# Performance work log

Hardware: AMD Instinct MI355X
Metric: run time of the kernel (lower is better)

The kernel has to match this reference:

```python
import jax, jax.numpy as jnp
import numpy as np

B, S, NX, H = 8, 1024, 1024, 16
HD = NX // H  # head dim = 64
MASKED_BIAS = -10000.0


def setup_inputs() -> dict:
    key = jax.random.key(0)
    ks = jax.random.split(key, 6)
    return {
        "x": jax.random.normal(ks[0], (B, S, NX), dtype=jnp.float32),
        "query": jax.random.normal(ks[1], (B, S, NX), dtype=jnp.float32),
        "c_attn_w": jax.random.normal(ks[2], (NX, 3 * NX), dtype=jnp.float32) * 0.02,
        "c_attn_b": jnp.zeros((3 * NX,), dtype=jnp.float32),
        "c_proj_w": jax.random.normal(ks[3], (NX, NX), dtype=jnp.float32) * 0.02,
        "c_proj_b": jnp.zeros((NX,), dtype=jnp.float32),
    }


def _split_heads(t):
    # [B, S, NX] -> [B, H, S, HD]
    b, s, _ = t.shape
    return t.reshape(b, s, H, HD).transpose(0, 2, 1, 3)


def reference(x, query, c_attn_w, c_attn_b, c_proj_w, c_proj_b):
    # Conv1D: y = x @ W + b
    kv = x @ c_attn_w + c_attn_b          # [B,S,3NX]; use key/value slices
    qy = query @ c_attn_w + c_attn_b      # [B,S,3NX]; use query slice
    q = _split_heads(qy[..., :NX])                     # [B,H,S,HD]
    k = _split_heads(kv[..., NX:2 * NX])               # [B,H,S,HD]
    v = _split_heads(kv[..., 2 * NX:])                 # [B,H,S,HD]

    w = jnp.einsum("bhqd,bhkd->bhqk", q, k) / jnp.sqrt(jnp.float32(HD))
    causal = jnp.tril(jnp.ones((S, S), dtype=bool))[None, None]
    w = jnp.where(causal, w, jnp.float32(MASKED_BIAS))
    w = jax.nn.softmax(w, axis=-1)
    a = jnp.einsum("bhqk,bhkd->bhqd", w, v)            # [B,H,S,HD]
    a = a.transpose(0, 2, 1, 3).reshape(B, S, NX)      # merge heads
    return a @ c_proj_w + c_proj_b
```

## Files before the change

kernel.cpp:

```cpp
#include <hip/hip_runtime.h>
#include <cstdint>
#include <cstddef>

#define Bb   8
#define Ss   1024
#define NXx  1024
#define Hh   16
#define HDd  64
#define Mm   (Bb*Ss)

typedef __bf16 bf16x8 __attribute__((ext_vector_type(8)));
typedef float  f32x4  __attribute__((ext_vector_type(4)));

__device__ __forceinline__ unsigned short f2bf(float f) {
    union { float f; unsigned int u; } v; v.f = f;
    return (unsigned short)((v.u + 0x8000u) >> 16);
}
__device__ __forceinline__ unsigned int f2bf_hi(float f) {
    union { float f; unsigned int u; } v; v.f = f;
    return (v.u + 0x8000u) & 0xffff0000u;
}

__device__ __forceinline__ void load_lds16(const unsigned short* g, unsigned short* lds_base) {
    __builtin_amdgcn_global_load_lds(
        (const __attribute__((address_space(1))) void*)g,
        (__attribute__((address_space(3))) void*)lds_base, 16, 0, 0);
}

__global__ __launch_bounds__(256) void prep(
    const float* __restrict__ x, const float* __restrict__ query,
    const float* __restrict__ caw, const float* __restrict__ cpw,
    unsigned short* __restrict__ xb, unsigned short* __restrict__ qb,
    unsigned short* __restrict__ Wt, unsigned short* __restrict__ Pt)
{
    __shared__ float tile[32][33];
    const int bid = blockIdx.x;
    const int tid = threadIdx.x;

    if (bid < 16384) {
        const float* in = (bid < 8192) ? x : query;
        unsigned short* out = (bid < 8192) ? xb : qb;
        const int i = ((bid & 8191) * 256 + tid) * 4;
        const float4 v = *(const float4*)(in + i);
        unsigned long long p = (unsigned long long)f2bf(v.x)
            | ((unsigned long long)f2bf(v.y) << 16)
            | ((unsigned long long)f2bf(v.z) << 32)
            | ((unsigned long long)f2bf(v.w) << 48);
        *(unsigned long long*)(out + i) = p;
        return;
    }

    const float* in;
    unsigned short* out;
    int C, t;
    if (bid < 16384 + 3072) { in = caw; out = Wt; C = 3072; t = bid - 16384; }
    else                    { in = cpw; out = Pt; C = 1024; t = bid - 19456; }
    const int ntx = C >> 5;
    const int c0 = (t % ntx) * 32, r0 = (t / ntx) * 32;
    const int tx = tid & 31, ty = tid >> 5;
    for (int i = ty; i < 32; i += 8)
        tile[i][tx] = in[(size_t)(r0 + i) * C + c0 + tx];
    __syncthreads();
    for (int i = ty; i < 32; i += 8)
        out[(size_t)(c0 + i) * 1024 + r0 + tx] = f2bf(tile[tx][i]);
}

__global__ __launch_bounds__(256) void gemm128(
    const unsigned short* __restrict__ Ax,
    const unsigned short* __restrict__ Aq,
    const unsigned short* __restrict__ Bt,
    const float* __restrict__ bias,
    int K, int mode,
    unsigned short* __restrict__ out_q,
    unsigned short* __restrict__ out_k,
    unsigned short* __restrict__ out_v,
    float* __restrict__ out_f)
{
    __shared__ unsigned short smem[16384];
    unsigned short (*As)[64] = (unsigned short (*)[64])(smem);
    unsigned short (*Bs)[64] = (unsigned short (*)[64])(smem + 8192);

    const int tid  = threadIdx.x;
    const int w    = tid >> 6;
    const int lane = tid & 63;

    const int nx   = (mode == 0) ? 24 : 8;
    const int nxh  = nx >> 1;
    const int n    = blockIdx.x;
    const int xcd  = n & 7;
    const int sgrp = n >> 3;
    const int m0   = ((xcd >> 1) * 16 + sgrp / nxh) * 128;
    const int n0   = ((xcd & 1) * nxh + sgrp % nxh) * 128;
    const int region = n0 >> 10;
    const unsigned short* A = (mode == 0 && region == 0) ? Aq : Ax;

    const int wm   = (w >> 1) * 64;
    const int wn   = (w & 1) * 64;
    const int lrow = lane & 15;
    const int quad = lane >> 4;

    f32x4 acc[4][4] = {};

    const int rr   = lane >> 3;
    const int scol = (((lane & 7) ^ (lane >> 3)) << 3);
    const unsigned short* Ag = A  + (size_t)(m0 + w * 32 + rr) * K + scol;
    const unsigned short* Bg = Bt + (size_t)(n0 + w * 32 + rr) * K + scol;
    unsigned short* ldsA = smem + (w * 32) * 64;
    unsigned short* ldsB = smem + 8192 + (w * 32) * 64;

    const int swz = lrow & 7;

    for (int k0 = 0; k0 < K; k0 += 64) {
        __syncthreads();
#pragma unroll
        for (int c = 0; c < 4; ++c) {
            load_lds16(Ag + (size_t)(c * 8) * K + k0, ldsA + c * 512);
            load_lds16(Bg + (size_t)(c * 8) * K + k0, ldsB + c * 512);
        }
        __syncthreads();
#pragma unroll
        for (int kk = 0; kk < 2; ++kk) {
            bf16x8 af[4], bfr[4];
            const int pc = (((kk * 4 + quad) ^ swz) << 3);
#pragma unroll
            for (int i = 0; i < 4; ++i) {
                af[i]  = *(const bf16x8*)&As[wm + i * 16 + lrow][pc];
                bfr[i] = *(const bf16x8*)&Bs[wn + i * 16 + lrow][pc];
            }
#pragma unroll
            for (int i = 0; i < 4; ++i)
#pragma unroll
                for (int j = 0; j < 4; ++j)
                    acc[i][j] = __builtin_amdgcn_mfma_f32_16x16x32_bf16(af[i], bfr[j], acc[i][j], 0, 0, 0);
        }
    }

    __syncthreads();

    if (mode == 1) {
#pragma unroll
        for (int i = 0; i < 4; ++i)
#pragma unroll
            for (int j = 0; j < 4; ++j) {
                const int ncol = n0 + wn + j * 16 + lrow;
                const float bv = bias[ncol];
#pragma unroll
                for (int r = 0; r < 4; ++r) {
                    const int mrow = m0 + wm + i * 16 + quad * 4 + r;
                    out_f[(size_t)mrow * NXx + ncol] = acc[i][j][r] + bv;
                }
            }
        return;
    }

    unsigned short* ep = smem + w * 2048;

    if (region != 2) {
        unsigned short* outp = (region == 0) ? out_q : out_k;
#pragma unroll
        for (int j = 0; j < 4; ++j) {
            const float bv = bias[n0 + wn + j * 16 + lrow];
#pragma unroll
            for (int i = 0; i < 4; ++i)
#pragma unroll
                for (int r = 0; r < 4; ++r)
                    ep[(i * 16 + quad * 4 + r) * 24 + lrow] = f2bf(acc[i][j][r] + bv);
#pragma unroll
            for (int t = 0; t < 2; ++t) {
                const int c    = t * 64 + lane;
                const int row  = c >> 1, ch = (c & 1) * 8;
                const int mrow = m0 + wm + row;
                const int cc   = (n0 + wn + j * 16 + ch) & (NXx - 1);
                const int hh   = cc >> 6, dd = cc & 63;
                const int bh   = (mrow >> 10) * Hh + hh;
                const int ss   = mrow & (Ss - 1);
                *(uint4*)&outp[((size_t)bh * Ss + ss) * HDd + dd] =
                    *(const uint4*)&ep[row * 24 + ch];
            }
        }
    } else {
#pragma unroll
        for (int j = 0; j < 4; ++j) {
            const float bv = bias[n0 + wn + j * 16 + lrow];
#pragma unroll
            for (int i = 0; i < 4; ++i)
#pragma unroll
                for (int r = 0; r < 4; ++r)
                    ep[lrow * 72 + i * 16 + quad * 4 + r] = f2bf(acc[i][j][r] + bv);
#pragma unroll
            for (int t = 0; t < 2; ++t) {
                const int c    = t * 64 + lane;
                const int col  = c >> 3, rc = (c & 7) * 8;
                const int cc   = (n0 + wn + j * 16 + col) & (NXx - 1);
                const int hh   = cc >> 6, dd = cc & 63;
                const int mrow = m0 + wm + rc;
                const int bh   = (mrow >> 10) * Hh + hh;
                const int ss   = mrow & (Ss - 1);
                *(uint4*)&out_v[((size_t)bh * HDd + dd) * Ss + ss] =
                    *(const uint4*)&ep[col * 72 + rc];
            }
        }
    }
}

__global__ __launch_bounds__(512, 4) void gemm256(
    const unsigned short* __restrict__ Ax,
    const unsigned short* __restrict__ Aq,
    const unsigned short* __restrict__ Bt,
    const float* __restrict__ bias,
    unsigned short* __restrict__ out_q,
    unsigned short* __restrict__ out_k,
    unsigned short* __restrict__ out_v)
{
    __shared__ unsigned short lds[36864];

    const int tid  = threadIdx.x;
    const int w    = tid >> 6;
    const int lane = tid & 63;
    const int wm   = (w >> 1) * 64;
    const int wn   = (w & 1) * 64;
    const int lrow = lane & 15;
    const int quad = lane >> 4;
    const int ph   = (quad ^ (lrow & 3) ^ (lrow >> 2)) & 3;

    const int n    = blockIdx.x;
    const int xcd  = n & 7;
    const int sg   = n >> 3;
    const int mi   = (xcd >> 1) * 8 + sg / 12;
    const int ni   = (xcd & 1) * 12 + sg % 12;
    const int m0   = mi << 8;
    const int n0   = ni << 7;
    const int region = n0 >> 10;
    const unsigned short* A = (region == 0) ? Aq : Ax;

    const int srow = lane >> 2;
    const int scol = (((lane & 3) ^ (srow & 3) ^ ((srow >> 2) & 3)) << 3);
    const unsigned short* pA0 = A  + (size_t)(m0 + w * 32 + srow) * 1024 + scol;
    const unsigned short* pA1 = A  + (size_t)(m0 + w * 32 + 16 + srow) * 1024 + scol;
    const unsigned short* pB0 = Bt + (size_t)(n0 + w * 16 + srow) * 1024 + scol;

    f32x4 acc[4][4] = {};

#pragma unroll
    for (int p = 0; p < 2; ++p) {
        const int bb = p * 12288;
        load_lds16(pA0, lds + bb + w * 1024);
        load_lds16(pA1, lds + bb + w * 1024 + 512);
        load_lds16(pB0, lds + bb + 8192 + w * 512);
        pA0 += 32; pA1 += 32; pB0 += 32;
    }

    int cbuf = 0;
    int sbuf = 2;
#pragma unroll 1
    for (int t = 0; t < 32; ++t) {
        __builtin_amdgcn_s_barrier();
        asm volatile("" ::: "memory");
        if (t <= 29) {
            const int bb = sbuf * 12288;
            load_lds16(pA0, lds + bb + w * 1024);
            load_lds16(pA1, lds + bb + w * 1024 + 512);
            load_lds16(pB0, lds + bb + 8192 + w * 512);
            pA0 += 32; pA1 += 32; pB0 += 32;
            asm volatile("s_waitcnt vmcnt(6)" ::: "memory");
        } else if (t == 30) {
            asm volatile("s_waitcnt vmcnt(3)" ::: "memory");
        } else {
            asm volatile("s_waitcnt vmcnt(0)" ::: "memory");
        }
        __builtin_amdgcn_s_barrier();
        asm volatile("" ::: "memory");

        const int rA = cbuf * 12288 + (wm + lrow) * 32 + ph * 8;
        const int rB = cbuf * 12288 + 8192 + (wn + lrow) * 32 + ph * 8;
        bf16x8 af[4], bq[4];
#pragma unroll
        for (int i = 0; i < 4; ++i) af[i] = *(const bf16x8*)&lds[rA + i * 512];
#pragma unroll
        for (int j = 0; j < 4; ++j) bq[j] = *(const bf16x8*)&lds[rB + j * 512];
        __builtin_amdgcn_s_setprio(1);
#pragma unroll
        for (int i = 0; i < 4; ++i)
#pragma unroll
            for (int j = 0; j < 4; ++j)
                acc[i][j] = __builtin_amdgcn_mfma_f32_16x16x32_bf16(af[i], bq[j], acc[i][j], 0, 0, 0);
        __builtin_amdgcn_s_setprio(0);

        cbuf = (cbuf == 2) ? 0 : cbuf + 1;
        sbuf = (sbuf == 2) ? 0 : sbuf + 1;
    }

    __syncthreads();

    unsigned short* ep = lds + w * 2048;

    if (region != 2) {
        unsigned short* outp = (region == 0) ? out_q : out_k;
#pragma unroll
        for (int j = 0; j < 4; ++j) {
            const float bv = bias[n0 + wn + j * 16 + lrow];
#pragma unroll
            for (int i = 0; i < 4; ++i)
#pragma unroll
                for (int r = 0; r < 4; ++r)
                    ep[(i * 16 + quad * 4 + r) * 24 + lrow] = f2bf(acc[i][j][r] + bv);
#pragma unroll
            for (int tt = 0; tt < 2; ++tt) {
                const int c    = tt * 64 + lane;
                const int row  = c >> 1, ch = (c & 1) * 8;
                const int mrow = m0 + wm + row;
                const int cc   = (n0 + wn + j * 16 + ch) & (NXx - 1);
                const int hh   = cc >> 6, dd = cc & 63;
                const int bh   = (mrow >> 10) * Hh + hh;
                const int ss   = mrow & (Ss - 1);
                *(uint4*)&outp[((size_t)bh * Ss + ss) * HDd + dd] =
                    *(const uint4*)&ep[row * 24 + ch];
            }
        }
    } else {
#pragma unroll
        for (int j = 0; j < 4; ++j) {
            const float bv = bias[n0 + wn + j * 16 + lrow];
#pragma unroll
            for (int i = 0; i < 4; ++i)
#pragma unroll
                for (int r = 0; r < 4; ++r)
                    ep[lrow * 72 + i * 16 + quad * 4 + r] = f2bf(acc[i][j][r] + bv);
#pragma unroll
            for (int tt = 0; tt < 2; ++tt) {
                const int c    = tt * 64 + lane;
                const int col  = c >> 3, rc = (c & 7) * 8;
                const int cc   = (n0 + wn + j * 16 + col) & (NXx - 1);
                const int hh   = cc >> 6, dd = cc & 63;
                const int mrow = m0 + wm + rc;
                const int bh   = (mrow >> 10) * Hh + hh;
                const int ss   = mrow & (Ss - 1);
                *(uint4*)&out_v[((size_t)bh * HDd + dd) * Ss + ss] =
                    *(const uint4*)&ep[col * 72 + rc];
            }
        }
    }
}

__global__ __launch_bounds__(256) void flash_attn(
    const unsigned short* __restrict__ Qh,
    const unsigned short* __restrict__ Kh,
    const unsigned short* __restrict__ Vt,
    unsigned short* __restrict__ about)
{
    __shared__ unsigned short Ks[64][64];
    __shared__ unsigned short Vs[64][64];
    __shared__ unsigned short Pl[4][32][72];

    const int tid  = threadIdx.x;
    const int w    = tid >> 6;
    const int lane = tid & 63;
    const int bh   = blockIdx.x & 127;
    const int pr   = blockIdx.x >> 7;
    const int b    = bh >> 4, h = bh & 15;
    const int lrow = lane & 15;
    const int quad = lane >> 4;

    const unsigned short* Qb = Qh + (size_t)bh * Ss * HDd;
    const unsigned short* Kb = Kh + (size_t)bh * Ss * HDd;
    const unsigned short* Vb = Vt + (size_t)bh * HDd * Ss;

    const int sr = lane >> 3;
    const int lc = (((lane & 7) ^ (lane >> 3)) << 3);
    unsigned short* ldsK0 = &Ks[w * 16][0];
    unsigned short* ldsK1 = &Ks[w * 16 + 8][0];
    unsigned short* ldsV0 = &Vs[w * 16][0];
    unsigned short* ldsV1 = &Vs[w * 16 + 8][0];

    const int swz = lrow & 7;
    const int ca = ((quad ^ swz) << 3);
    const int cb = (((4 + quad) ^ swz) << 3);

    for (int half = 0; half < 2; ++half) {
        const int qt = half ? (7 - pr) : pr;
        const int qw = qt * 128 + w * 32;

        bf16x8 aq[2][2];
#pragma unroll
        for (int g = 0; g < 2; ++g)
#pragma unroll
            for (int c = 0; c < 2; ++c)
                aq[g][c] = *(const bf16x8*)(Qb + (size_t)(qw + g * 16 + lrow) * HDd + c * 32 + quad * 8);

        f32x4 O[2][4] = {};
        float lsum[2] = { 0.f, 0.f };

        const int nkt = 2 * qt + 2;
        for (int kt = 0; kt < nkt; ++kt) {
            const int k0 = kt * 64;

            __syncthreads();
            load_lds16(Kb + (size_t)(k0 + w * 16 + sr) * HDd + lc,     ldsK0);
            load_lds16(Kb + (size_t)(k0 + w * 16 + sr + 8) * HDd + lc, ldsK1);
            load_lds16(Vb + (size_t)(w * 16 + sr) * Ss + k0 + lc,      ldsV0);
            load_lds16(Vb + (size_t)(w * 16 + sr + 8) * Ss + k0 + lc,  ldsV1);
            __syncthreads();

            if (k0 > qw + 31) continue;

            f32x4 st[2][4] = {};
#pragma unroll
            for (int j = 0; j < 4; ++j) {
                const bf16x8 kf0 = *(const bf16x8*)&Ks[j * 16 + lrow][ca];
                const bf16x8 kf1 = *(const bf16x8*)&Ks[j * 16 + lrow][cb];
                st[0][j] = __builtin_amdgcn_mfma_f32_16x16x32_bf16(kf0, aq[0][0], st[0][j], 0, 0, 0);
                st[0][j] = __builtin_amdgcn_mfma_f32_16x16x32_bf16(kf1, aq[0][1], st[0][j], 0, 0, 0);
                st[1][j] = __builtin_amdgcn_mfma_f32_16x16x32_bf16(kf0, aq[1][0], st[1][j], 0, 0, 0);
                st[1][j] = __builtin_amdgcn_mfma_f32_16x16x32_bf16(kf1, aq[1][1], st[1][j], 0, 0, 0);
            }

            const bool needMask = (k0 + 63 > qw);
#pragma unroll
            for (int g = 0; g < 2; ++g) {
                const int qg = qw + g * 16 + lrow;
#pragma unroll
                for (int j = 0; j < 4; ++j) {
                    const int kbase = k0 + j * 16 + quad * 4;
                    float e0 = __expf(st[g][j][0] * 0.125f);
                    float e1 = __expf(st[g][j][1] * 0.125f);
                    float e2 = __expf(st[g][j][2] * 0.125f);
                    float e3 = __expf(st[g][j][3] * 0.125f);
                    if (needMask) {
                        if (kbase     > qg) e0 = 0.f;
                        if (kbase + 1 > qg) e1 = 0.f;
                        if (kbase + 2 > qg) e2 = 0.f;
                        if (kbase + 3 > qg) e3 = 0.f;
                    }
                    lsum[g] += (e0 + e1) + (e2 + e3);
                    uint2 pk;
                    pk.x = (unsigned)f2bf(e0) | f2bf_hi(e1);
                    pk.y = (unsigned)f2bf(e2) | f2bf_hi(e3);
                    *(uint2*)&Pl[w][g * 16 + lrow][j * 16 + quad * 4] = pk;
                }
            }

            bf16x8 ap[2][2];
#pragma unroll
            for (int g = 0; g < 2; ++g)
#pragma unroll
                for (int c = 0; c < 2; ++c)
                    ap[g][c] = *(const bf16x8*)&Pl[w][g * 16 + lrow][c * 32 + quad * 8];
#pragma unroll
            for (int f = 0; f < 4; ++f) {
                const bf16x8 vf0 = *(const bf16x8*)&Vs[f * 16 + lrow][ca];
                const bf16x8 vf1 = *(const bf16x8*)&Vs[f * 16 + lrow][cb];
                O[0][f] = __builtin_amdgcn_mfma_f32_16x16x32_bf16(ap[0][0], vf0, O[0][f], 0, 0, 0);
                O[0][f] = __builtin_amdgcn_mfma_f32_16x16x32_bf16(ap[0][1], vf1, O[0][f], 0, 0, 0);
                O[1][f] = __builtin_amdgcn_mfma_f32_16x16x32_bf16(ap[1][0], vf0, O[1][f], 0, 0, 0);
                O[1][f] = __builtin_amdgcn_mfma_f32_16x16x32_bf16(ap[1][1], vf1, O[1][f], 0, 0, 0);
            }
        }

#pragma unroll
        for (int g = 0; g < 2; ++g) {
            float l = lsum[g];
            l += __shfl_xor(l, 16);
            l += __shfl_xor(l, 32);
            const float inv = 1.0f / l;
#pragma unroll
            for (int r = 0; r < 4; ++r) {
                const float invr = __shfl(inv, quad * 4 + r);
                const int q = qw + g * 16 + quad * 4 + r;
                const size_t base = ((size_t)b * Ss + q) * NXx + h * HDd;
#pragma unroll
                for (int f = 0; f < 4; ++f)
                    about[base + f * 16 + lrow] = f2bf(O[g][f][r] * invr);
            }
        }
    }
}

extern "C" void kernel_launch(void* const* d_in, const int* in_sizes, int n_in,
                              void* d_out, int out_size, void* d_ws, size_t ws_size,
                              hipStream_t stream) {
    const float* x        = (const float*)d_in[0];
    const float* query    = (const float*)d_in[1];
    const float* c_attn_w = (const float*)d_in[2];
    const float* c_attn_b = (const float*)d_in[3];
    const float* c_proj_w = (const float*)d_in[4];
    const float* c_proj_b = (const float*)d_in[5];
    float* out = (float*)d_out;

    const size_t nTok = (size_t)Mm * NXx;
    char* ws = (char*)d_ws;
    unsigned short* xb    = (unsigned short*)ws;                 ws += nTok * 2;
    unsigned short* qb    = (unsigned short*)ws;                 ws += nTok * 2;
    unsigned short* Wt    = (unsigned short*)ws;                 ws += (size_t)3 * NXx * NXx * 2;
    unsigned short* Pt    = (unsigned short*)ws;                 ws += (size_t)NXx * NXx * 2;
    unsigned short* Qh    = (unsigned short*)ws;                 ws += nTok * 2;
    unsigned short* Kh    = (unsigned short*)ws;                 ws += nTok * 2;
    unsigned short* Vt    = (unsigned short*)ws;                 ws += nTok * 2;
    unsigned short* about = (unsigned short*)ws;                 ws += nTok * 2;
    if ((size_t)(ws - (char*)d_ws) > ws_size) return;

    prep<<<20480, 256, 0, stream>>>(x, query, c_attn_w, c_proj_w, xb, qb, Wt, Pt);

    gemm256<<<768, 512, 0, stream>>>(xb, qb, Wt, c_attn_b, Qh, Kh, Vt);

    flash_attn<<<512, 256, 0, stream>>>(Qh, Kh, Vt, about);

    gemm128<<<dim3(8 * 64), 256, 0, stream>>>(about, nullptr, Pt, c_proj_b, NXx, 1,
                                              nullptr, nullptr, nullptr, out);
}
```

Measured before the change: 259.3 us.

## Double-buffer K/V tiles in flash attention and shrink GEMM to two LDS stages

The attention kernel now merges its two query-tile passes into one flat loop of 18 K/V tiles. It double-buffers K and V in LDS and prefetches the next tile with async global-to-LDS loads while computing the current one, instead of using a synchronous load between two barriers. The QKV GEMM drops from a triple-buffered to a double-buffered LDS pipeline, which cuts LDS use so the occupancy hint can rise from 4 to 6. The trade-off is less prefetch depth in the GEMM in exchange for more resident blocks, plus extra control logic in attention to flush outputs and switch query tiles mid-loop.

```diff
diff --git a/kernel.cpp b/kernel.cpp
--- a/kernel.cpp
+++ b/kernel.cpp
@@ -203,7 +203,7 @@
     }
 }
 
-__global__ __launch_bounds__(512, 4) void gemm256(
+__global__ __launch_bounds__(512, 6) void gemm256(
     const unsigned short* __restrict__ Ax,
     const unsigned short* __restrict__ Aq,
     const unsigned short* __restrict__ Bt,
@@ -212,7 +212,7 @@
     unsigned short* __restrict__ out_k,
     unsigned short* __restrict__ out_v)
 {
-    __shared__ unsigned short lds[36864];
+    __shared__ unsigned short lds[24576];
 
     const int tid  = threadIdx.x;
     const int w    = tid >> 6;
@@ -241,29 +241,21 @@
 
     f32x4 acc[4][4] = {};
 
-#pragma unroll
-    for (int p = 0; p < 2; ++p) {
-        const int bb = p * 12288;
-        load_lds16(pA0, lds + bb + w * 1024);
-        load_lds16(pA1, lds + bb + w * 1024 + 512);
-        load_lds16(pB0, lds + bb + 8192 + w * 512);
-        pA0 += 32; pA1 += 32; pB0 += 32;
-    }
-
-    int cbuf = 0;
-    int sbuf = 2;
+    load_lds16(pA0, lds + w * 1024);
+    load_lds16(pA1, lds + w * 1024 + 512);
+    load_lds16(pB0, lds + 8192 + w * 512);
+    pA0 += 32; pA1 += 32; pB0 += 32;
+
 #pragma unroll 1
     for (int t = 0; t < 32; ++t) {
         __builtin_amdgcn_s_barrier();
         asm volatile("" ::: "memory");
-        if (t <= 29) {
-            const int bb = sbuf * 12288;
+        if (t < 31) {
+            const int bb = ((t + 1) & 1) * 12288;
             load_lds16(pA0, lds + bb + w * 1024);
             load_lds16(pA1, lds + bb + w * 1024 + 512);
             load_lds16(pB0, lds + bb + 8192 + w * 512);
             pA0 += 32; pA1 += 32; pB0 += 32;
-            asm volatile("s_waitcnt vmcnt(6)" ::: "memory");
-        } else if (t == 30) {
             asm volatile("s_waitcnt vmcnt(3)" ::: "memory");
         } else {
             asm volatile("s_waitcnt vmcnt(0)" ::: "memory");
@@ -271,8 +263,9 @@
         __builtin_amdgcn_s_barrier();
         asm volatile("" ::: "memory");
 
-        const int rA = cbuf * 12288 + (wm + lrow) * 32 + ph * 8;
-        const int rB = cbuf * 12288 + 8192 + (wn + lrow) * 32 + ph * 8;
+        const int base = (t & 1) * 12288;
+        const int rA = base + (wm + lrow) * 32 + ph * 8;
+        const int rB = base + 8192 + (wn + lrow) * 32 + ph * 8;
         bf16x8 af[4], bq[4];
 #pragma unroll
         for (int i = 0; i < 4; ++i) af[i] = *(const bf16x8*)&lds[rA + i * 512];
@@ -285,9 +278,6 @@
             for (int j = 0; j < 4; ++j)
                 acc[i][j] = __builtin_amdgcn_mfma_f32_16x16x32_bf16(af[i], bq[j], acc[i][j], 0, 0, 0);
         __builtin_amdgcn_s_setprio(0);
-
-        cbuf = (cbuf == 2) ? 0 : cbuf + 1;
-        sbuf = (sbuf == 2) ? 0 : sbuf + 1;
     }
 
     __syncthreads();
@@ -348,8 +338,8 @@
     const unsigned short* __restrict__ Vt,
     unsigned short* __restrict__ about)
 {
-    __shared__ unsigned short Ks[64][64];
-    __shared__ unsigned short Vs[64][64];
+    __shared__ unsigned short Ks[2][64][64];
+    __shared__ unsigned short Vs[2][64][64];
     __shared__ unsigned short Pl[4][32][72];
 
     const int tid  = threadIdx.x;
@@ -367,110 +357,152 @@
 
     const int sr = lane >> 3;
     const int lc = (((lane & 7) ^ (lane >> 3)) << 3);
-    unsigned short* ldsK0 = &Ks[w * 16][0];
-    unsigned short* ldsK1 = &Ks[w * 16 + 8][0];
-    unsigned short* ldsV0 = &Vs[w * 16][0];
-    unsigned short* ldsV1 = &Vs[w * 16 + 8][0];
 
     const int swz = lrow & 7;
     const int ca = ((quad ^ swz) << 3);
     const int cb = (((4 + quad) ^ swz) << 3);
 
-    for (int half = 0; half < 2; ++half) {
-        const int qt = half ? (7 - pr) : pr;
-        const int qw = qt * 128 + w * 32;
-
-        bf16x8 aq[2][2];
+    const int nkt0 = 2 * pr + 2;
+    int qt = pr;
+    int qw = qt * 128 + w * 32;
+
+    bf16x8 aq[2][2];
+#pragma unroll
+    for (int g = 0; g < 2; ++g)
+#pragma unroll
+        for (int c = 0; c < 2; ++c)
+            aq[g][c] = *(const bf16x8*)(Qb + (size_t)(qw + g * 16 + lrow) * HDd + c * 32 + quad * 8);
+
+    f32x4 O[2][4] = {};
+    float lsum[2] = { 0.f, 0.f };
+
+    load_lds16(Kb + (size_t)(w * 16 + sr) * HDd + lc,     &Ks[0][w * 16][0]);
+    load_lds16(Kb + (size_t)(w * 16 + sr + 8) * HDd + lc, &Ks[0][w * 16 + 8][0]);
+    load_lds16(Vb + (size_t)(w * 16 + sr) * Ss + lc,      &Vs[0][w * 16][0]);
+    load_lds16(Vb + (size_t)(w * 16 + sr + 8) * Ss + lc,  &Vs[0][w * 16 + 8][0]);
+
+#pragma unroll 1
+    for (int it = 0; it < 18; ++it) {
+        __builtin_amdgcn_s_barrier();
+        asm volatile("" ::: "memory");
+        if (it < 17) {
+            const int itn  = it + 1;
+            const int bsel = itn & 1;
+            const int k0n  = (itn >= nkt0 ? itn - nkt0 : itn) * 64;
+            load_lds16(Kb + (size_t)(k0n + w * 16 + sr) * HDd + lc,     &Ks[bsel][w * 16][0]);
+            load_lds16(Kb + (size_t)(k0n + w * 16 + sr + 8) * HDd + lc, &Ks[bsel][w * 16 + 8][0]);
+            load_lds16(Vb + (size_t)(w * 16 + sr) * Ss + k0n + lc,      &Vs[bsel][w * 16][0]);
+            load_lds16(Vb + (size_t)(w * 16 + sr + 8) * Ss + k0n + lc,  &Vs[bsel][w * 16 + 8][0]);
+            asm volatile("s_waitcnt vmcnt(4)" ::: "memory");
+        } else {
+            asm volatile("s_waitcnt vmcnt(0)" ::: "memory");
+        }
+        __builtin_amdgcn_s_barrier();
+        asm volatile("" ::: "memory");
+
+        if (it == nkt0) {
+#pragma unroll
+            for (int g = 0; g < 2; ++g) {
+                float l = lsum[g];
+                l += __shfl_xor(l, 16);
+                l += __shfl_xor(l, 32);
+                const float inv = 1.0f / l;
+#pragma unroll
+                for (int r = 0; r < 4; ++r) {
+                    const float invr = __shfl(inv, quad * 4 + r);
+                    const int q = qw + g * 16 + quad * 4 + r;
+                    const size_t base = ((size_t)b * Ss + q) * NXx + h * HDd;
+#pragma unroll
+                    for (int f = 0; f < 4; ++f)
+                        about[base + f * 16 + lrow] = f2bf(O[g][f][r] * invr);
+                }
+            }
+            qt = 7 - pr;
+            qw = qt * 128 + w * 32;
+#pragma unroll
+            for (int g = 0; g < 2; ++g)
+#pragma unroll
+                for (int c = 0; c < 2; ++c)
+                    aq[g][c] = *(const bf16x8*)(Qb + (size_t)(qw + g * 16 + lrow) * HDd + c * 32 + quad * 8);
+#pragma unroll
+            for (int g = 0; g < 2; ++g) {
+                lsum[g] = 0.f;
+#pragma unroll
+                for (int f = 0; f < 4; ++f) O[g][f] = (f32x4){0.f, 0.f, 0.f, 0.f};
+            }
+        }
+
+        const int k0 = (it >= nkt0 ? it - nkt0 : it) * 64;
+        if (k0 > qw + 31) continue;
+        const int bs = it & 1;
+
+        f32x4 st[2][4] = {};
+#pragma unroll
+        for (int j = 0; j < 4; ++j) {
+            const bf16x8 kf0 = *(const bf16x8*)&Ks[bs][j * 16 + lrow][ca];
+            const bf16x8 kf1 = *(const bf16x8*)&Ks[bs][j * 16 + lrow][cb];
+            st[0][j] = __builtin_amdgcn_mfma_f32_16x16x32_bf16(kf0, aq[0][0], st[0][j], 0, 0, 0);
+            st[0][j] = __builtin_amdgcn_mfma_f32_16x16x32_bf16(kf1, aq[0][1], st[0][j], 0, 0, 0);
+            st[1][j] = __builtin_amdgcn_mfma_f32_16x16x32_bf16(kf0, aq[1][0], st[1][j], 0, 0, 0);
+            st[1][j] = __builtin_amdgcn_mfma_f32_16x16x32_bf16(kf1, aq[1][1], st[1][j], 0, 0, 0);
+        }
+
+        const bool needMask = (k0 + 63 > qw);
+#pragma unroll
+        for (int g = 0; g < 2; ++g) {
+            const int qg = qw + g * 16 + lrow;
+#pragma unroll
+            for (int j = 0; j < 4; ++j) {
+                const int kbase = k0 + j * 16 + quad * 4;
+                float e0 = __expf(st[g][j][0] * 0.125f);
+                float e1 = __expf(st[g][j][1] * 0.125f);
+                float e2 = __expf(st[g][j][2] * 0.125f);
+                float e3 = __expf(st[g][j][3] * 0.125f);
+                if (needMask) {
+                    if (kbase     > qg) e0 = 0.f;
+                    if (kbase + 1 > qg) e1 = 0.f;
+                    if (kbase + 2 > qg) e2 = 0.f;
+                    if (kbase + 3 > qg) e3 = 0.f;
+                }
+                lsum[g] += (e0 + e1) + (e2 + e3);
+                uint2 pk;
+                pk.x = (unsigned)f2bf(e0) | f2bf_hi(e1);
+                pk.y = (unsigned)f2bf(e2) | f2bf_hi(e3);
+                *(uint2*)&Pl[w][g * 16 + lrow][j * 16 + quad * 4] = pk;
+            }
+        }
+
+        bf16x8 ap[2][2];
 #pragma unroll
         for (int g = 0; g < 2; ++g)
 #pragma unroll
             for (int c = 0; c < 2; ++c)
-                aq[g][c] = *(const bf16x8*)(Qb + (size_t)(qw + g * 16 + lrow) * HDd + c * 32 + quad * 8);
-
-        f32x4 O[2][4] = {};
-        float lsum[2] = { 0.f, 0.f };
-
-        const int nkt = 2 * qt + 2;
-        for (int kt = 0; kt < nkt; ++kt) {
-            const int k0 = kt * 64;
-
-            __syncthreads();
-            load_lds16(Kb + (size_t)(k0 + w * 16 + sr) * HDd + lc,     ldsK0);
-            load_lds16(Kb + (size_t)(k0 + w * 16 + sr + 8) * HDd + lc, ldsK1);
-            load_lds16(Vb + (size_t)(w * 16 + sr) * Ss + k0 + lc,      ldsV0);
-            load_lds16(Vb + (size_t)(w * 16 + sr + 8) * Ss + k0 + lc,  ldsV1);
-            __syncthreads();
-
-            if (k0 > qw + 31) continue;
-
-            f32x4 st[2][4] = {};
-#pragma unroll
-            for (int j = 0; j < 4; ++j) {
-                const bf16x8 kf0 = *(const bf16x8*)&Ks[j * 16 + lrow][ca];
-                const bf16x8 kf1 = *(const bf16x8*)&Ks[j * 16 + lrow][cb];
-                st[0][j] = __builtin_amdgcn_mfma_f32_16x16x32_bf16(kf0, aq[0][0], st[0][j], 0, 0, 0);
-                st[0][j] = __builtin_amdgcn_mfma_f32_16x16x32_bf16(kf1, aq[0][1], st[0][j], 0, 0, 0);
-                st[1][j] = __builtin_amdgcn_mfma_f32_16x16x32_bf16(kf0, aq[1][0], st[1][j], 0, 0, 0);
-                st[1][j] = __builtin_amdgcn_mfma_f32_16x16x32_bf16(kf1, aq[1][1], st[1][j], 0, 0, 0);
-            }
-
-            const bool needMask = (k0 + 63 > qw);
-#pragma unroll
-            for (int g = 0; g < 2; ++g) {
-                const int qg = qw + g * 16 + lrow;
-#pragma unroll
-                for (int j = 0; j < 4; ++j) {
-                    const int kbase = k0 + j * 16 + quad * 4;
-                    float e0 = __expf(st[g][j][0] * 0.125f);
-                    float e1 = __expf(st[g][j][1] * 0.125f);
-                    float e2 = __expf(st[g][j][2] * 0.125f);
-                    float e3 = __expf(st[g][j][3] * 0.125f);
-                    if (needMask) {
-                        if (kbase     > qg) e0 = 0.f;
-                        if (kbase + 1 > qg) e1 = 0.f;
-                        if (kbase + 2 > qg) e2 = 0.f;
-                        if (kbase + 3 > qg) e3 = 0.f;
-                    }
-                    lsum[g] += (e0 + e1) + (e2 + e3);
-                    uint2 pk;
-                    pk.x = (unsigned)f2bf(e0) | f2bf_hi(e1);
-                    pk.y = (unsigned)f2bf(e2) | f2bf_hi(e3);
-                    *(uint2*)&Pl[w][g * 16 + lrow][j * 16 + quad * 4] = pk;
-                }
-            }
-
-            bf16x8 ap[2][2];
-#pragma unroll
-            for (int g = 0; g < 2; ++g)
-#pragma unroll
-                for (int c = 0; c < 2; ++c)
-                    ap[g][c] = *(const bf16x8*)&Pl[w][g * 16 + lrow][c * 32 + quad * 8];
-#pragma unroll
-            for (int f = 0; f < 4; ++f) {
-                const bf16x8 vf0 = *(const bf16x8*)&Vs[f * 16 + lrow][ca];
-                const bf16x8 vf1 = *(const bf16x8*)&Vs[f * 16 + lrow][cb];
-                O[0][f] = __builtin_amdgcn_mfma_f32_16x16x32_bf16(ap[0][0], vf0, O[0][f], 0, 0, 0);
-                O[0][f] = __builtin_amdgcn_mfma_f32_16x16x32_bf16(ap[0][1], vf1, O[0][f], 0, 0, 0);
-                O[1][f] = __builtin_amdgcn_mfma_f32_16x16x32_bf16(ap[1][0], vf0, O[1][f], 0, 0, 0);
-                O[1][f] = __builtin_amdgcn_mfma_f32_16x16x32_bf16(ap[1][1], vf1, O[1][f], 0, 0, 0);
-            }
-        }
-
-#pragma unroll
-        for (int g = 0; g < 2; ++g) {
-            float l = lsum[g];
-            l += __shfl_xor(l, 16);
-            l += __shfl_xor(l, 32);
-            const float inv = 1.0f / l;
-#pragma unroll
-            for (int r = 0; r < 4; ++r) {
-                const float invr = __shfl(inv, quad * 4 + r);
-                const int q = qw + g * 16 + quad * 4 + r;
-                const size_t base = ((size_t)b * Ss + q) * NXx + h * HDd;
-#pragma unroll
-                for (int f = 0; f < 4; ++f)
-                    about[base + f * 16 + lrow] = f2bf(O[g][f][r] * invr);
-            }
+                ap[g][c] = *(const bf16x8*)&Pl[w][g * 16 + lrow][c * 32 + quad * 8];
+#pragma unroll
+        for (int f = 0; f < 4; ++f) {
+            const bf16x8 vf0 = *(const bf16x8*)&Vs[bs][f * 16 + lrow][ca];
+            const bf16x8 vf1 = *(const bf16x8*)&Vs[bs][f * 16 + lrow][cb];
+            O[0][f] = __builtin_amdgcn_mfma_f32_16x16x32_bf16(ap[0][0], vf0, O[0][f], 0, 0, 0);
+            O[0][f] = __builtin_amdgcn_mfma_f32_16x16x32_bf16(ap[0][1], vf1, O[0][f], 0, 0, 0);
+            O[1][f] = __builtin_amdgcn_mfma_f32_16x16x32_bf16(ap[1][0], vf0, O[1][f], 0, 0, 0);
+            O[1][f] = __builtin_amdgcn_mfma_f32_16x16x32_bf16(ap[1][1], vf1, O[1][f], 0, 0, 0);
+        }
+    }
+
+#pragma unroll
+    for (int g = 0; g < 2; ++g) {
+        float l = lsum[g];
+        l += __shfl_xor(l, 16);
+        l += __shfl_xor(l, 32);
+        const float inv = 1.0f / l;
+#pragma unroll
+        for (int r = 0; r < 4; ++r) {
+            const float invr = __shfl(inv, quad * 4 + r);
+            const int q = qw + g * 16 + quad * 4 + r;
+            const size_t base = ((size_t)b * Ss + q) * NXx + h * HDd;
+#pragma unroll
+            for (int f = 0; f < 4; ++f)
+                about[base + f * 16 + lrow] = f2bf(O[g][f][r] * invr);
         }
     }
 }
```

Result: slower. 720.5 us (+177.9%).
